# Optimization experiments

Hardware: AMD Instinct MI355X
Metric: run time of the kernel (lower is better)

## Reference

```python
import jax, jax.numpy as jnp
import numpy as np

HEADS = 4
DIM_HEAD = 32


def setup_inputs() -> dict:
    key = jax.random.key(0)
    k1, k2, k3, k4, k5 = jax.random.split(key, 5)
    dim = 128
    hidden = HEADS * DIM_HEAD  # 128
    h = w = 384
    x = jax.random.normal(k1, (1, dim, h, w), dtype=jnp.float32)
    # 1x1 conv weights (eqx Conv2d layout: [out_c, in_c, 1, 1]) + biases
    w_qkv = jax.random.normal(k2, (3 * hidden, dim, 1, 1), dtype=jnp.float32) * (1.0 / np.sqrt(dim))
    b_qkv = jax.random.normal(k3, (3 * hidden,), dtype=jnp.float32) * 0.01
    w_out = jax.random.normal(k4, (dim, hidden, 1, 1), dtype=jnp.float32) * (1.0 / np.sqrt(hidden))
    b_out = jax.random.normal(k5, (dim,), dtype=jnp.float32) * 0.01
    return {"x": x, "w_qkv": w_qkv, "b_qkv": b_qkv, "w_out": w_out, "b_out": b_out}


def reference(x, w_qkv, b_qkv, w_out, b_out):
    b, c, h, w = x.shape  # b == 1 (module squeezes batch)
    xs = x[0]  # (c, h, w)
    # 1x1 conv == channel matmul
    qkv = jnp.einsum('oc,chw->ohw', w_qkv[:, :, 0, 0], xs) + b_qkv[:, None, None]
    # rearrange '(qkv heads c) h w -> qkv heads c (h w)'
    qkv = qkv.reshape(3, HEADS, DIM_HEAD, h * w)
    q, k, v = qkv[0], qkv[1], qkv[2]  # each (heads, d, n)
    k = jax.nn.softmax(k, axis=-1)
    # context: (heads, d, e) -- small per-head outer product accumulated over n
    context = jnp.einsum('hdn,hen->hde', k, v)
    out = jnp.einsum('hde,hdn->hen', context, q)  # (heads, e, n)
    out = out.reshape(HEADS * DIM_HEAD, h, w)
    y = jnp.einsum('oc,chw->ohw', w_out[:, :, 0, 0], out) + b_out[:, None, None]
    return y  # (dim, h, w) -- module returns squeezed output
```

## Files before the change

kernel.cpp:

```cpp
#include <hip/hip_runtime.h>
#include <hip/hip_bf16.h>
#include <stdint.h>


#define NPOS 147456
#define NTILES 2304
#define NB1 768

typedef __attribute__((ext_vector_type(8))) short short8;
typedef __attribute__((ext_vector_type(4))) float floatx4;

__device__ __forceinline__ uint16_t f2bf(float f) {
    uint32_t u = __float_as_uint(f);
    return (uint16_t)((u + 0x7fffu + ((u >> 16) & 1u)) >> 16);
}
__device__ __forceinline__ uint32_t pack2(float a, float b) {
    return (uint32_t)f2bf(a) | ((uint32_t)f2bf(b) << 16);
}

#define XS_STRIDE 68
#define PS_STRIDE 36

__global__ __launch_bounds__(256, 3) void k1_ctx(
    const float* __restrict__ x, const float* __restrict__ w_qkv,
    const float* __restrict__ b_qkv, float* __restrict__ cpart, int nb1)
{
    __shared__ uint32_t Xs[64 * XS_STRIDE];
    __shared__ uint32_t Ps[256 * PS_STRIDE];

    const int t = threadIdx.x;
    const int lane = t & 63;
    const int wavu = __builtin_amdgcn_readfirstlane(t >> 6);
    const int m = lane & 15, quad = lane >> 4;
    const int kvbase = wavu * 64;
    const bool is_k = (wavu < 2);

    short8 wfr[4][4];
    float biasv[4];
    #pragma unroll
    for (int kt = 0; kt < 4; ++kt) {
        const int row = 128 + kvbase + kt * 16 + m;
        biasv[kt] = b_qkv[row];
        #pragma unroll
        for (int ks = 0; ks < 4; ++ks) {
            const float* p = w_qkv + row * 128 + ks * 32 + quad * 8;
            short8 w;
            #pragma unroll
            for (int j = 0; j < 8; ++j) w[j] = (short)f2bf(p[j]);
            wfr[kt][ks] = w;
        }
    }

    floatx4 acc2[4];
    #pragma unroll
    for (int i = 0; i < 4; ++i) acc2[i] = (floatx4){0.f, 0.f, 0.f, 0.f};
    float sacc[4] = {0.f, 0.f, 0.f, 0.f};

    for (int tile = blockIdx.x; tile < NTILES; tile += nb1) {
        const int n0 = tile * 64;
        {
            const int c0 = wavu * 32;
            #pragma unroll
            for (int i = 0; i < 8; ++i) {
                const int c = c0 + i * 4;
                const float* xp = x + (size_t)c * NPOS + n0 + lane;
                float a0 = xp[0];
                float a1 = xp[NPOS];
                float a2 = xp[2 * NPOS];
                float a3 = xp[3 * NPOS];
                uint2 w; w.x = pack2(a0, a1); w.y = pack2(a2, a3);
                *(uint2*)&Xs[lane * XS_STRIDE + c / 2] = w;
            }
        }
        __syncthreads();
        #pragma unroll
        for (int nt = 0; nt < 4; ++nt) {
            short8 afr[4];
            #pragma unroll
            for (int ks = 0; ks < 4; ++ks)
                afr[ks] = *(const short8*)&Xs[(nt * 16 + m) * XS_STRIDE + ks * 16 + quad * 4];
            floatx4 pa[4];
            #pragma unroll
            for (int kt = 0; kt < 4; ++kt) pa[kt] = (floatx4){0.f, 0.f, 0.f, 0.f};
            #pragma unroll
            for (int ks = 0; ks < 4; ++ks)
                #pragma unroll
                for (int kt = 0; kt < 4; ++kt)
                    pa[kt] = __builtin_amdgcn_mfma_f32_16x16x32_bf16(afr[ks], wfr[kt][ks], pa[kt], 0, 0, 0);
            #pragma unroll
            for (int kt = 0; kt < 4; ++kt) {
                float v0 = pa[kt][0] + biasv[kt];
                float v1 = pa[kt][1] + biasv[kt];
                float v2 = pa[kt][2] + biasv[kt];
                float v3 = pa[kt][3] + biasv[kt];
                if (is_k) {
                    v0 = __expf(v0); v1 = __expf(v1);
                    v2 = __expf(v2); v3 = __expf(v3);
                    sacc[kt] += (v0 + v1) + (v2 + v3);
                }
                uint2 w; w.x = pack2(v0, v1); w.y = pack2(v2, v3);
                const int kvrow = kvbase + kt * 16 + m;
                *(uint2*)&Ps[kvrow * PS_STRIDE + nt * 8 + quad * 2] = w;
            }
        }
        __syncthreads();
        #pragma unroll
        for (int ks = 0; ks < 2; ++ks) {
            short8 ea[2], vb[2];
            #pragma unroll
            for (int dt = 0; dt < 2; ++dt)
                ea[dt] = *(const short8*)&Ps[(wavu * 32 + dt * 16 + m) * PS_STRIDE + ks * 16 + quad * 4];
            #pragma unroll
            for (int et = 0; et < 2; ++et)
                vb[et] = *(const short8*)&Ps[(128 + wavu * 32 + et * 16 + m) * PS_STRIDE + ks * 16 + quad * 4];
            #pragma unroll
            for (int dt = 0; dt < 2; ++dt)
                #pragma unroll
                for (int et = 0; et < 2; ++et)
                    acc2[dt * 2 + et] = __builtin_amdgcn_mfma_f32_16x16x32_bf16(ea[dt], vb[et], acc2[dt * 2 + et], 0, 0, 0);
        }
    }
    float* __restrict__ dst = cpart + (size_t)blockIdx.x * 4224;
    #pragma unroll
    for (int dt = 0; dt < 2; ++dt)
        #pragma unroll
        for (int et = 0; et < 2; ++et)
            #pragma unroll
            for (int r = 0; r < 4; ++r) {
                const int d = dt * 16 + quad * 4 + r, e = et * 16 + m;
                dst[wavu * 1024 + d * 32 + e] = acc2[dt * 2 + et][r];
            }
    if (is_k) {
        #pragma unroll
        for (int kt = 0; kt < 4; ++kt) {
            float s = sacc[kt];
            s += __shfl_down(s, 32, 64);
            s += __shfl_down(s, 16, 64);
            if (lane < 16) dst[4096 + kvbase + kt * 16 + lane] = s;
        }
    }
}

__global__ void k2a(const float* __restrict__ cpart, float* __restrict__ ctxU, int nb1)
{
    const int u = blockIdx.x * 256 + threadIdx.x;
    if (u >= 4224 * 8) return;
    const int j = u % 4224, p = u / 4224;
    float s = 0.f;
    for (int b = p; b < nb1; b += 8) s += cpart[(size_t)b * 4224 + j];
    atomicAdd(&ctxU[j], s);
}

__global__ void k2b(const float* __restrict__ w_out, const float* __restrict__ ctxU,
                    float* __restrict__ A)
{
    const int tg = blockIdx.x * 256 + threadIdx.x;
    const int o = tg >> 7, hd = tg & 127, h = hd >> 5;
    float s = 0.f;
    #pragma unroll
    for (int e = 0; e < 32; ++e)
        s = fmaf(w_out[o * 128 + h * 32 + e], ctxU[hd * 32 + e], s);
    A[tg] = s / ctxU[4096 + hd];
}

__global__ void k2c(const float* __restrict__ A, const float* __restrict__ w_qkv,
                    const float* __restrict__ b_qkv, const float* __restrict__ b_out,
                    float* __restrict__ Bm, float* __restrict__ cvec)
{
    const int tg = blockIdx.x * 256 + threadIdx.x;
    const int o = tg >> 7, c = tg & 127;
    float s = 0.f;
    #pragma unroll 8
    for (int hd = 0; hd < 128; ++hd)
        s = fmaf(A[o * 128 + hd], w_qkv[hd * 128 + c], s);
    Bm[tg] = s;
    if (tg < 128) {
        float cs = b_out[tg];
        for (int hd = 0; hd < 128; ++hd) cs = fmaf(A[tg * 128 + hd], b_qkv[hd], cs);
        cvec[tg] = cs;
    }
}

__global__ __launch_bounds__(256) void k3(
    const float* __restrict__ x, const float* __restrict__ Bm,
    const float* __restrict__ cvec, float* __restrict__ y)
{
    __shared__ uint32_t Xs[64 * XS_STRIDE];
    const int t = threadIdx.x, lane = t & 63;
    const int wavu = __builtin_amdgcn_readfirstlane(t >> 6);
    const int m = lane & 15, quad = lane >> 4;
    const int n0 = blockIdx.x * 64;

    short8 bfr[2][4];
    float cv[2];
    #pragma unroll
    for (int ot = 0; ot < 2; ++ot) {
        const int o = (wavu * 2 + ot) * 16 + m;
        cv[ot] = cvec[o];
        #pragma unroll
        for (int ks = 0; ks < 4; ++ks) {
            const float* p = Bm + o * 128 + ks * 32 + quad * 8;
            short8 w;
            #pragma unroll
            for (int j = 0; j < 8; ++j) w[j] = (short)f2bf(p[j]);
            bfr[ot][ks] = w;
        }
    }
    {
        const int c0 = wavu * 32;
        #pragma unroll
        for (int i = 0; i < 8; ++i) {
            const int c = c0 + i * 4;
            const float* xp = x + (size_t)c * NPOS + n0 + lane;
            float a0 = xp[0];
            float a1 = xp[NPOS];
            float a2 = xp[2 * NPOS];
            float a3 = xp[3 * NPOS];
            uint2 w; w.x = pack2(a0, a1); w.y = pack2(a2, a3);
            *(uint2*)&Xs[lane * XS_STRIDE + c / 2] = w;
        }
    }
    __syncthreads();
    floatx4 acc[2][4];
    #pragma unroll
    for (int ot = 0; ot < 2; ++ot)
        #pragma unroll
        for (int nt = 0; nt < 4; ++nt) acc[ot][nt] = (floatx4){0.f, 0.f, 0.f, 0.f};
    #pragma unroll
    for (int nt = 0; nt < 4; ++nt) {
        short8 afr[4];
        #pragma unroll
        for (int ks = 0; ks < 4; ++ks)
            afr[ks] = *(const short8*)&Xs[(nt * 16 + m) * XS_STRIDE + ks * 16 + quad * 4];
        #pragma unroll
        for (int ks = 0; ks < 4; ++ks)
            #pragma unroll
            for (int ot = 0; ot < 2; ++ot)
                acc[ot][nt] = __builtin_amdgcn_mfma_f32_16x16x32_bf16(afr[ks], bfr[ot][ks], acc[ot][nt], 0, 0, 0);
    }
    #pragma unroll
    for (int ot = 0; ot < 2; ++ot) {
        const int o = (wavu * 2 + ot) * 16 + m;
        #pragma unroll
        for (int nt = 0; nt < 4; ++nt) {
            floatx4 v = acc[ot][nt];
            v.x += cv[ot]; v.y += cv[ot]; v.z += cv[ot]; v.w += cv[ot];
            *(floatx4*)(y + (size_t)o * NPOS + n0 + nt * 16 + quad * 4) = v;
        }
    }
}

extern "C" void kernel_launch(void* const* d_in, const int* in_sizes, int n_in,
                              void* d_out, int out_size, void* d_ws, size_t ws_size,
                              hipStream_t stream)
{
    const float* x     = (const float*)d_in[0];
    const float* w_qkv = (const float*)d_in[1];
    const float* b_qkv = (const float*)d_in[2];
    const float* w_out = (const float*)d_in[3];
    const float* b_out = (const float*)d_in[4];
    float* y = (float*)d_out;

    const size_t tail = (4224 + 16384 + 16384 + 128) * 4;
    int nb1 = NB1;
    if (ws_size < tail + (size_t)nb1 * 16896) {
        long cap = ((long)ws_size - (long)tail) / 16896;
        nb1 = (int)cap;
        if (nb1 < 1) nb1 = 1;
        if (nb1 > NB1) nb1 = NB1;
    }
    char* wsb = (char*)d_ws;
    float* cpart = (float*)wsb;
    float* ctxU  = (float*)(wsb + (size_t)nb1 * 16896);
    float* A     = ctxU + 4224;
    float* Bm    = A + 16384;
    float* cvec  = Bm + 16384;

    hipLaunchKernelGGL(k1_ctx, dim3(nb1), dim3(256), 0, stream, x, w_qkv, b_qkv, cpart, nb1);
    hipMemsetAsync(ctxU, 0, 16896, stream);
    hipLaunchKernelGGL(k2a, dim3(132), dim3(256), 0, stream, cpart, ctxU, nb1);
    hipLaunchKernelGGL(k2b, dim3(64), dim3(256), 0, stream, w_out, ctxU, A);
    hipLaunchKernelGGL(k2c, dim3(64), dim3(256), 0, stream, A, w_qkv, b_qkv, b_out, Bm, cvec);
    hipLaunchKernelGGL(k3, dim3(NTILES), dim3(256), 0, stream, x, Bm, cvec, y);
}
```

Measured before the change: 217.7 us.

## Double-buffer x tiles in context kernel, fuse reduction kernels, use packed bf16 convert

The context kernel now prefetches the next x tile into registers while computing the current one, then writes it into a second LDS buffer. This is meant to hide global load latency. It also lowers the block count and occupancy target. The memset, atomic reduction and two small GEMV kernels are replaced by partial stores plus one fused k2bc kernel, cutting launches and atomics. A hardware packed bf16 conversion builtin is used when available, and k3 batches its x loads into registers first.

```diff
diff --git a/kernel.cpp b/kernel.cpp
--- a/kernel.cpp
+++ b/kernel.cpp
@@ -5,7 +5,7 @@
 
 #define NPOS 147456
 #define NTILES 2304
-#define NB1 768
+#define NB1 512
 
 typedef __attribute__((ext_vector_type(8))) short short8;
 typedef __attribute__((ext_vector_type(4))) float floatx4;
@@ -15,17 +15,23 @@
     return (uint16_t)((u + 0x7fffu + ((u >> 16) & 1u)) >> 16);
 }
 __device__ __forceinline__ uint32_t pack2(float a, float b) {
+#if __has_builtin(__builtin_amdgcn_cvt_pk_bf16_f32)
+    auto r = __builtin_amdgcn_cvt_pk_bf16_f32(a, b);
+    uint32_t u; __builtin_memcpy(&u, &r, sizeof(u));
+    return u;
+#else
     return (uint32_t)f2bf(a) | ((uint32_t)f2bf(b) << 16);
+#endif
 }
 
 #define XS_STRIDE 68
 #define PS_STRIDE 36
 
-__global__ __launch_bounds__(256, 3) void k1_ctx(
+__global__ __launch_bounds__(256, 2) void k1_ctx(
     const float* __restrict__ x, const float* __restrict__ w_qkv,
     const float* __restrict__ b_qkv, float* __restrict__ cpart, int nb1)
 {
-    __shared__ uint32_t Xs[64 * XS_STRIDE];
+    __shared__ uint32_t Xs[2][64 * XS_STRIDE];
     __shared__ uint32_t Ps[256 * PS_STRIDE];
 
     const int t = threadIdx.x;
@@ -34,6 +40,7 @@
     const int m = lane & 15, quad = lane >> 4;
     const int kvbase = wavu * 64;
     const bool is_k = (wavu < 2);
+    const int c0 = wavu * 32;
 
     short8 wfr[4][4];
     float biasv[4];
@@ -56,29 +63,38 @@
     for (int i = 0; i < 4; ++i) acc2[i] = (floatx4){0.f, 0.f, 0.f, 0.f};
     float sacc[4] = {0.f, 0.f, 0.f, 0.f};
 
+    {
+        const int nofs = blockIdx.x * 64 + lane;
+        float pf[32];
+        #pragma unroll
+        for (int i = 0; i < 32; ++i)
+            pf[i] = x[(c0 + i) * NPOS + nofs];
+        #pragma unroll
+        for (int i = 0; i < 8; ++i) {
+            uint2 w;
+            w.x = pack2(pf[i * 4 + 0], pf[i * 4 + 1]);
+            w.y = pack2(pf[i * 4 + 2], pf[i * 4 + 3]);
+            *(uint2*)&Xs[0][lane * XS_STRIDE + (c0 + i * 4) / 2] = w;
+        }
+    }
+    __syncthreads();
+
+    int cur = 0;
     for (int tile = blockIdx.x; tile < NTILES; tile += nb1) {
-        const int n0 = tile * 64;
-        {
-            const int c0 = wavu * 32;
-            #pragma unroll
-            for (int i = 0; i < 8; ++i) {
-                const int c = c0 + i * 4;
-                const float* xp = x + (size_t)c * NPOS + n0 + lane;
-                float a0 = xp[0];
-                float a1 = xp[NPOS];
-                float a2 = xp[2 * NPOS];
-                float a3 = xp[3 * NPOS];
-                uint2 w; w.x = pack2(a0, a1); w.y = pack2(a2, a3);
-                *(uint2*)&Xs[lane * XS_STRIDE + c / 2] = w;
-            }
-        }
-        __syncthreads();
+        const int tn = tile + nb1;
+        float pf[32];
+        if (tn < NTILES) {
+            const int nofs = tn * 64 + lane;
+            #pragma unroll
+            for (int i = 0; i < 32; ++i)
+                pf[i] = x[(c0 + i) * NPOS + nofs];
+        }
         #pragma unroll
         for (int nt = 0; nt < 4; ++nt) {
             short8 afr[4];
             #pragma unroll
             for (int ks = 0; ks < 4; ++ks)
-                afr[ks] = *(const short8*)&Xs[(nt * 16 + m) * XS_STRIDE + ks * 16 + quad * 4];
+                afr[ks] = *(const short8*)&Xs[cur][(nt * 16 + m) * XS_STRIDE + ks * 16 + quad * 4];
             floatx4 pa[4];
             #pragma unroll
             for (int kt = 0; kt < 4; ++kt) pa[kt] = (floatx4){0.f, 0.f, 0.f, 0.f};
@@ -98,7 +114,9 @@
                     v2 = __expf(v2); v3 = __expf(v3);
                     sacc[kt] += (v0 + v1) + (v2 + v3);
                 }
-                uint2 w; w.x = pack2(v0, v1); w.y = pack2(v2, v3);
+                uint2 w;
+                w.x = pack2(v0, v1);
+                w.y = pack2(v2, v3);
                 const int kvrow = kvbase + kt * 16 + m;
                 *(uint2*)&Ps[kvrow * PS_STRIDE + nt * 8 + quad * 2] = w;
             }
@@ -119,6 +137,17 @@
                 for (int et = 0; et < 2; ++et)
                     acc2[dt * 2 + et] = __builtin_amdgcn_mfma_f32_16x16x32_bf16(ea[dt], vb[et], acc2[dt * 2 + et], 0, 0, 0);
         }
+        if (tn < NTILES) {
+            #pragma unroll
+            for (int i = 0; i < 8; ++i) {
+                uint2 w;
+                w.x = pack2(pf[i * 4 + 0], pf[i * 4 + 1]);
+                w.y = pack2(pf[i * 4 + 2], pf[i * 4 + 3]);
+                *(uint2*)&Xs[cur ^ 1][lane * XS_STRIDE + (c0 + i * 4) / 2] = w;
+            }
+        }
+        __syncthreads();
+        cur ^= 1;
     }
     float* __restrict__ dst = cpart + (size_t)blockIdx.x * 4224;
     #pragma unroll
@@ -141,43 +170,57 @@
     }
 }
 
-__global__ void k2a(const float* __restrict__ cpart, float* __restrict__ ctxU, int nb1)
+__global__ void k2a(const float* __restrict__ cpart, float* __restrict__ ctxP, int nb1)
 {
     const int u = blockIdx.x * 256 + threadIdx.x;
     if (u >= 4224 * 8) return;
     const int j = u % 4224, p = u / 4224;
     float s = 0.f;
     for (int b = p; b < nb1; b += 8) s += cpart[(size_t)b * 4224 + j];
-    atomicAdd(&ctxU[j], s);
-}
-
-__global__ void k2b(const float* __restrict__ w_out, const float* __restrict__ ctxU,
-                    float* __restrict__ A)
-{
-    const int tg = blockIdx.x * 256 + threadIdx.x;
-    const int o = tg >> 7, hd = tg & 127, h = hd >> 5;
-    float s = 0.f;
-    #pragma unroll
-    for (int e = 0; e < 32; ++e)
-        s = fmaf(w_out[o * 128 + h * 32 + e], ctxU[hd * 32 + e], s);
-    A[tg] = s / ctxU[4096 + hd];
-}
-
-__global__ void k2c(const float* __restrict__ A, const float* __restrict__ w_qkv,
-                    const float* __restrict__ b_qkv, const float* __restrict__ b_out,
-                    float* __restrict__ Bm, float* __restrict__ cvec)
-{
-    const int tg = blockIdx.x * 256 + threadIdx.x;
-    const int o = tg >> 7, c = tg & 127;
-    float s = 0.f;
-    #pragma unroll 8
-    for (int hd = 0; hd < 128; ++hd)
-        s = fmaf(A[o * 128 + hd], w_qkv[hd * 128 + c], s);
-    Bm[tg] = s;
-    if (tg < 128) {
-        float cs = b_out[tg];
-        for (int hd = 0; hd < 128; ++hd) cs = fmaf(A[tg * 128 + hd], b_qkv[hd], cs);
-        cvec[tg] = cs;
+    ctxP[p * 4224 + j] = s;
+}
+
+__global__ __launch_bounds__(128) void k2bc(
+    const float* __restrict__ ctxP, const float* __restrict__ w_out,
+    const float* __restrict__ w_qkv, const float* __restrict__ b_qkv,
+    const float* __restrict__ b_out, float* __restrict__ Bm, float* __restrict__ cvec)
+{
+    __shared__ float ctx33[128 * 33];
+    __shared__ float Ss[128];
+    __shared__ float Arow[128];
+    __shared__ float red[128];
+    const int o = blockIdx.x, t = threadIdx.x;
+    for (int j = t; j < 4224; j += 128) {
+        float s = 0.f;
+        #pragma unroll
+        for (int p = 0; p < 8; ++p) s += ctxP[p * 4224 + j];
+        if (j < 4096) ctx33[(j >> 5) * 33 + (j & 31)] = s;
+        else          Ss[j - 4096] = s;
+    }
+    __syncthreads();
+    {
+        const int h = t >> 5;
+        float s = 0.f;
+        #pragma unroll
+        for (int e = 0; e < 32; ++e)
+            s = fmaf(w_out[o * 128 + h * 32 + e], ctx33[t * 33 + e], s);
+        Arow[t] = s / Ss[t];
+    }
+    __syncthreads();
+    {
+        float s = 0.f;
+        #pragma unroll 16
+        for (int hd = 0; hd < 128; ++hd)
+            s = fmaf(Arow[hd], w_qkv[hd * 128 + t], s);
+        Bm[o * 128 + t] = s;
+    }
+    red[t] = Arow[t] * b_qkv[t];
+    __syncthreads();
+    if (t == 0) {
+        float cs = b_out[o];
+        #pragma unroll 8
+        for (int i = 0; i < 128; ++i) cs += red[i];
+        cvec[o] = cs;
     }
 }
 
@@ -190,6 +233,7 @@
     const int wavu = __builtin_amdgcn_readfirstlane(t >> 6);
     const int m = lane & 15, quad = lane >> 4;
     const int n0 = blockIdx.x * 64;
+    const int c0 = wavu * 32;
 
     short8 bfr[2][4];
     float cv[2];
@@ -207,17 +251,17 @@
         }
     }
     {
-        const int c0 = wavu * 32;
+        const int nofs = n0 + lane;
+        float pf[32];
+        #pragma unroll
+        for (int i = 0; i < 32; ++i)
+            pf[i] = x[(c0 + i) * NPOS + nofs];
         #pragma unroll
         for (int i = 0; i < 8; ++i) {
-            const int c = c0 + i * 4;
-            const float* xp = x + (size_t)c * NPOS + n0 + lane;
-            float a0 = xp[0];
-            float a1 = xp[NPOS];
-            float a2 = xp[2 * NPOS];
-            float a3 = xp[3 * NPOS];
-            uint2 w; w.x = pack2(a0, a1); w.y = pack2(a2, a3);
-            *(uint2*)&Xs[lane * XS_STRIDE + c / 2] = w;
+            uint2 w;
+            w.x = pack2(pf[i * 4 + 0], pf[i * 4 + 1]);
+            w.y = pack2(pf[i * 4 + 2], pf[i * 4 + 3]);
+            *(uint2*)&Xs[lane * XS_STRIDE + (c0 + i * 4) / 2] = w;
         }
     }
     __syncthreads();
@@ -261,7 +305,7 @@
     const float* b_out = (const float*)d_in[4];
     float* y = (float*)d_out;
 
-    const size_t tail = (4224 + 16384 + 16384 + 128) * 4;
+    const size_t tail = (size_t)(8 * 4224 + 16384 + 128) * 4;
     int nb1 = NB1;
     if (ws_size < tail + (size_t)nb1 * 16896) {
         long cap = ((long)ws_size - (long)tail) / 16896;
@@ -271,15 +315,12 @@
     }
     char* wsb = (char*)d_ws;
     float* cpart = (float*)wsb;
-    float* ctxU  = (float*)(wsb + (size_t)nb1 * 16896);
-    float* A     = ctxU + 4224;
-    float* Bm    = A + 16384;
+    float* ctxP  = (float*)(wsb + (size_t)nb1 * 16896);
+    float* Bm    = ctxP + 8 * 4224;
     float* cvec  = Bm + 16384;
 
     hipLaunchKernelGGL(k1_ctx, dim3(nb1), dim3(256), 0, stream, x, w_qkv, b_qkv, cpart, nb1);
-    hipMemsetAsync(ctxU, 0, 16896, stream);
-    hipLaunchKernelGGL(k2a, dim3(132), dim3(256), 0, stream, cpart, ctxU, nb1);
-    hipLaunchKernelGGL(k2b, dim3(64), dim3(256), 0, stream, w_out, ctxU, A);
-    hipLaunchKernelGGL(k2c, dim3(64), dim3(256), 0, stream, A, w_qkv, b_qkv, b_out, Bm, cvec);
+    hipLaunchKernelGGL(k2a, dim3(132), dim3(256), 0, stream, cpart, ctxP, nb1);
+    hipLaunchKernelGGL(k2bc, dim3(128), dim3(128), 0, stream, ctxP, w_out, w_qkv, b_qkv, b_out, Bm, cvec);
     hipLaunchKernelGGL(k3, dim3(NTILES), dim3(256), 0, stream, x, Bm, cvec, y);
 }
```

New measurement: 206.2 us. -5.3%, faster.
